# Kernel tuning notes

Hardware: AMD Instinct MI355X
Metric: run time of the kernel (lower is better)

Reference implementation:

```python
import jax, jax.numpy as jnp
import numpy as np

SCALE = 10.0
TEMP = 0.5
SIM_TH = 0.7
EPOCH = 1
KL_WEIGHT = max(0.5 * (1 - EPOCH / 60), 0.1)
NEG_INF = -1e30


def _normalize(x, eps=1e-12):
    n = jnp.linalg.norm(x, axis=-1, keepdims=True)
    return x / jnp.maximum(n, eps)


def setup_inputs() -> dict:
    key = jax.random.key(0)
    ks = jax.random.split(key, 6)
    P, B, D, N, K = 4, 128, 512, 32768, 10
    # 0.02 scale keeps pairwise distances O(1) so exp(-SCALE*dist) does not underflow
    feature = jax.random.normal(ks[0], (P, B, D), jnp.float32) * 0.02
    text_feature = jax.random.normal(ks[1], (B, P, D), jnp.float32) * 0.02
    centers = jax.random.normal(ks[2], (P, N, D), jnp.float32) * 0.02
    position = jax.random.randint(ks[3], (B,), 0, N)
    cross_indices = jax.random.randint(ks[4], (B, K), 0, N)
    vid = jax.random.randint(ks[5], (N,), 0, 751)
    return {"feature": feature, "text_feature": text_feature, "centers": centers,
            "position": position, "cross_indices": cross_indices, "vid": vid}


def _align_loss(feature, text_feature):
    # feature: [P,B,D]; text_feature: [B,P,D] (detached in original)
    img = _normalize(feature)
    txt = _normalize(jax.lax.stop_gradient(jnp.transpose(text_feature, (1, 0, 2))))
    img_sim = jnp.einsum('pbd,pcd->pbc', img, img) / TEMP   # [P,B,B]
    txt_sim = jnp.einsum('pbd,pcd->pbc', txt, txt) / TEMP
    mask = (img_sim > SIM_TH) & (txt_sim > SIM_TH)
    valid = mask.any(-1)                                   # [P,B] row/col validity
    colm = valid[:, None, :]                               # mask over columns
    il = jnp.where(colm, img_sim, NEG_INF)
    tl = jnp.where(colm, txt_sim, NEG_INF)
    img_logp = jax.nn.log_softmax(il, -1)
    txt_logp = jax.nn.log_softmax(tl, -1)                  # fully detached (txt detached)
    txt_prob = jnp.exp(txt_logp)
    img_logp_sg = jax.lax.stop_gradient(img_logp)
    img_prob = jnp.exp(img_logp_sg)
    # F.kl_div(input=log q, target=p) = sum p*(log p - log q), batchmean over valid rows
    kl1 = jnp.sum(jnp.where(colm, txt_prob * (txt_logp - img_logp), 0.0), -1)      # [P,B]
    kl2 = jnp.sum(jnp.where(colm, img_prob * (img_logp_sg - txt_logp), 0.0), -1)
    nvalid = valid.sum(-1)                                 # [P]
    r1 = jnp.sum(jnp.where(valid, kl1, 0.0), -1)
    r2 = jnp.sum(jnp.where(valid, kl2, 0.0), -1)
    per_part = 0.5 * (r1 + r2) / jnp.maximum(nvalid, 1)
    return jnp.sum(jnp.where(nvalid > 0, per_part, 0.0))


def _contrastive_loss(feature, centers, position, cross_indices):
    P, B, D = feature.shape
    N = centers.shape[1]
    pos_feats = jnp.take(centers, cross_indices, axis=1)   # [P,B,K,D]
    fn2 = jnp.sum(feature * feature, -1)                   # [P,B]
    pn2 = jnp.sum(pos_feats * pos_feats, -1)               # [P,B,K]
    pd2 = fn2[..., None] + pn2 - 2.0 * jnp.einsum('pbd,pbkd->pbk', feature, pos_feats)
    pos_dist = jnp.sqrt(jnp.maximum(pd2, 1e-12))           # [P,B,K]
    cn2 = jnp.sum(centers * centers, -1)                   # [P,N]
    nd2 = fn2[..., None] + cn2[:, None, :] - 2.0 * jnp.einsum('pbd,pnd->pbn', feature, centers)
    neg_dist = jnp.sqrt(jnp.maximum(nd2, 1e-12))           # [P,B,N]
    neg_mask = (jnp.ones((N,), bool)
                .at[cross_indices.reshape(-1)].set(False)
                .at[position].set(False))
    x = jnp.log(jnp.sum(jnp.exp(-SCALE * pos_dist), -1))   # [P,B]
    ey = jnp.exp(-SCALE * neg_dist) * neg_mask[None, None, :].astype(neg_dist.dtype)
    y = jnp.log(jnp.sum(ey, -1))                           # [P,B]
    l = jnp.sum(y - x, -1) / B                             # per-part, div by feature.size(1)
    l = jnp.where(jnp.isnan(l), 0.0, l)
    return jnp.sum(l) / P


def reference(feature, text_feature, centers, position, cross_indices, vid):
    align_loss = _align_loss(feature, text_feature)
    contrastive_loss = _contrastive_loss(feature, centers, position, cross_indices)
    total_loss = contrastive_loss + KL_WEIGHT * align_loss
    pos_vid = jnp.take(vid, cross_indices, axis=0)         # [B,K]
    return total_loss, contrastive_loss, align_loss, pos_vid
```

## Files before the change

### kernel.cpp

```cpp
#include <hip/hip_runtime.h>
#include <hip/hip_bf16.h>
#include <math.h>

#define P_ 4
#define B_ 128
#define D_ 512
#define N_ 32768
#define K_ 10
#define TNB 128
#define NT2 (N_ / TNB)
#define BK2 32
#define NCH (D_ / BK2)
#define KP2 42

typedef __attribute__((ext_vector_type(8))) short bf16x8;
typedef __attribute__((ext_vector_type(4))) float f32x4;

#define LDS_BARRIER() asm volatile("s_waitcnt lgkmcnt(0)\n\ts_barrier" ::: "memory")

static __device__ __forceinline__ float block_sum_128(float v, float* sh) {
    const int t = threadIdx.x;
    sh[t] = v; __syncthreads();
    #pragma unroll
    for (int s = 64; s > 0; s >>= 1) { if (t < s) sh[t] += sh[t + s]; __syncthreads(); }
    float r = sh[0]; __syncthreads();
    return r;
}

static __device__ __forceinline__ uint2 pack_bf16x4(float4 v) {
    union { __hip_bfloat162 h; unsigned u; } lo, hi;
    lo.h = __float22bfloat162_rn(make_float2(v.x, v.y));
    hi.h = __float22bfloat162_rn(make_float2(v.z, v.w));
    uint2 r; r.x = lo.u; r.y = hi.u;
    return r;
}

__global__ __launch_bounds__(256) void prep_kernel(const float* __restrict__ feature,
                                                   unsigned short* __restrict__ Abf,
                                                   float* __restrict__ fn2) {
    const int pb = blockIdx.x;
    const int t = threadIdx.x;
    const float2 v = *(const float2*)(feature + (size_t)pb * D_ + 2 * t);
    union { __hip_bfloat162 h; unsigned u; } pk;
    pk.h = __float22bfloat162_rn(make_float2(v.x, v.y));
    ((unsigned*)Abf)[(size_t)pb * (D_ / 2) + t] = pk.u;
    __shared__ float sred[256];
    sred[t] = v.x * v.x + v.y * v.y;
    __syncthreads();
    #pragma unroll
    for (int s = 128; s > 0; s >>= 1) { if (t < s) sred[t] += sred[t + s]; __syncthreads(); }
    if (t == 0) fn2[pb] = sred[0];
}

__global__ __launch_bounds__(128) void sim_kernel(
    const float* __restrict__ feature,
    const float* __restrict__ text_feature,
    float* __restrict__ img_sim,
    float* __restrict__ txt_sim,
    float* __restrict__ validf,
    float* __restrict__ Ssum) {
    const int p = blockIdx.x;
    const int b0 = blockIdx.y * 2;
    const int c = threadIdx.x;
    if (blockIdx.y == 0) Ssum[p * B_ + c] = 0.0f;
    __shared__ float ai[2][D_];
    __shared__ float at[2][D_];
    __shared__ float cinv_i[128];
    __shared__ float cinv_t[128];
    __shared__ int flags[2];
    #pragma unroll
    for (int i = 0; i < 8; ++i) {
        int idx = c + i * 128;
        int row = idx >> 9, d = idx & 511;
        ai[row][d] = feature[(size_t)(p * B_ + b0 + row) * D_ + d];
        at[row][d] = text_feature[((size_t)(b0 + row) * P_ + p) * D_ + d];
    }
    if (c < 2) flags[c] = 0;
    __syncthreads();
    float di[2] = {0, 0};
    float dt[2] = {0, 0};
    float ssi = 0.0f, sst = 0.0f;
    const float* fc = feature + (size_t)(p * B_ + c) * D_;
    const float* tc = text_feature + ((size_t)c * P_ + p) * D_;
    for (int d = 0; d < D_; d += 4) {
        float4 vi = *(const float4*)(fc + d);
        float4 vt = *(const float4*)(tc + d);
        ssi += vi.x * vi.x + vi.y * vi.y + vi.z * vi.z + vi.w * vi.w;
        sst += vt.x * vt.x + vt.y * vt.y + vt.z * vt.z + vt.w * vt.w;
        #pragma unroll
        for (int i = 0; i < 2; ++i) {
            float4 a4 = *(const float4*)&ai[i][d];
            float4 t4 = *(const float4*)&at[i][d];
            di[i] += a4.x * vi.x + a4.y * vi.y + a4.z * vi.z + a4.w * vi.w;
            dt[i] += t4.x * vt.x + t4.y * vt.y + t4.z * vt.z + t4.w * vt.w;
        }
    }
    cinv_i[c] = 1.0f / fmaxf(sqrtf(ssi), 1e-12f);
    cinv_t[c] = 1.0f / fmaxf(sqrtf(sst), 1e-12f);
    __syncthreads();
    #pragma unroll
    for (int i = 0; i < 2; ++i) {
        float is = 2.0f * di[i] * cinv_i[b0 + i] * cinv_i[c];
        float ts = 2.0f * dt[i] * cinv_t[b0 + i] * cinv_t[c];
        img_sim[(size_t)(p * B_ + b0 + i) * B_ + c] = is;
        txt_sim[(size_t)(p * B_ + b0 + i) * B_ + c] = ts;
        if (is > 0.7f && ts > 0.7f) flags[i] = 1;
    }
    __syncthreads();
    if (c < 2) validf[p * B_ + b0 + c] = (float)flags[c];
}

__global__ __launch_bounds__(256) void kl_kernel(
    const float* __restrict__ img_sim,
    const float* __restrict__ txt_sim,
    const float* __restrict__ validf,
    float* __restrict__ klrow) {
    const int l = threadIdx.x & 63;
    const int wv = threadIdx.x >> 6;
    const int p = blockIdx.x;
    const int r = blockIdx.y * 4 + wv;
    const size_t base = (size_t)(p * B_ + r) * B_;
    const bool v0 = validf[p * B_ + l] > 0.5f;
    const bool v1 = validf[p * B_ + 64 + l] > 0.5f;
    const float il0 = v0 ? img_sim[base + l] : -1e30f;
    const float il1 = v1 ? img_sim[base + 64 + l] : -1e30f;
    const float tl0 = v0 ? txt_sim[base + l] : -1e30f;
    const float tl1 = v1 ? txt_sim[base + 64 + l] : -1e30f;
    float mi = fmaxf(il0, il1), mt = fmaxf(tl0, tl1);
    #pragma unroll
    for (int off = 32; off > 0; off >>= 1) {
        mi = fmaxf(mi, __shfl_xor(mi, off));
        mt = fmaxf(mt, __shfl_xor(mt, off));
    }
    float si = expf(il0 - mi) + expf(il1 - mi);
    float st = expf(tl0 - mt) + expf(tl1 - mt);
    #pragma unroll
    for (int off = 32; off > 0; off >>= 1) {
        si += __shfl_xor(si, off);
        st += __shfl_xor(st, off);
    }
    const float lsei = mi + logf(si);
    const float lset = mt + logf(st);
    float term = 0.0f;
    if (v0) {
        float lpi = il0 - lsei, lpt = tl0 - lset;
        term += expf(lpt) * (lpt - lpi) + expf(lpi) * (lpi - lpt);
    }
    if (v1) {
        float lpi = il1 - lsei, lpt = tl1 - lset;
        term += expf(lpt) * (lpt - lpi) + expf(lpi) * (lpi - lpt);
    }
    #pragma unroll
    for (int off = 32; off > 0; off >>= 1) term += __shfl_xor(term, off);
    if (l == 0) klrow[p * B_ + r] = (validf[p * B_ + r] > 0.5f) ? term : 0.0f;
}

__global__ void posx_kernel(const float* __restrict__ feature,
                            const float* __restrict__ centers,
                            const int* __restrict__ cross,
                            float* __restrict__ xarr) {
    const int pb = blockIdx.x;
    const int p = pb >> 7, b = pb & 127;
    const int l = threadIdx.x;
    const float* f = feature + (size_t)pb * D_;
    float4 f0 = *(const float4*)(f + l * 4);
    float4 f1 = *(const float4*)(f + 256 + l * 4);
    float fs = f0.x * f0.x + f0.y * f0.y + f0.z * f0.z + f0.w * f0.w
             + f1.x * f1.x + f1.y * f1.y + f1.z * f1.z + f1.w * f1.w;
    #pragma unroll
    for (int off = 32; off > 0; off >>= 1) fs += __shfl_down(fs, off);
    float ex = 0.0f;
    #pragma unroll
    for (int k = 0; k < K_; ++k) {
        int idx = cross[b * K_ + k];
        const float* cp = centers + ((size_t)p * N_ + idx) * D_;
        float4 c0 = *(const float4*)(cp + l * 4);
        float4 c1 = *(const float4*)(cp + 256 + l * 4);
        float dot = f0.x * c0.x + f0.y * c0.y + f0.z * c0.z + f0.w * c0.w
                  + f1.x * c1.x + f1.y * c1.y + f1.z * c1.z + f1.w * c1.w;
        float pn2 = c0.x * c0.x + c0.y * c0.y + c0.z * c0.z + c0.w * c0.w
                  + c1.x * c1.x + c1.y * c1.y + c1.z * c1.z + c1.w * c1.w;
        #pragma unroll
        for (int off = 32; off > 0; off >>= 1) {
            dot += __shfl_down(dot, off);
            pn2 += __shfl_down(pn2, off);
        }
        if (l == 0) {
            float d2 = fs + pn2 - 2.0f * dot;
            ex += expf(-10.0f * sqrtf(fmaxf(d2, 1e-12f)));
        }
    }
    if (l == 0) xarr[pb] = logf(ex);
}

__global__ __launch_bounds__(256) void neg_mfma_kernel(
    const unsigned short* __restrict__ Abf,
    const float* __restrict__ centers,
    const float* __restrict__ fn2,
    const int* __restrict__ cross,
    const int* __restrict__ position,
    float* __restrict__ Ssum) {
    const int tile = blockIdx.x;
    const int p = blockIdx.y;
    const int n0g = tile * TNB;
    const int t = threadIdx.x;
    const int l = t & 63;
    const int w = t >> 6;
    const int m0w = (w & 1) * 64;
    const int n0w = (w >> 1) * 64;

    __shared__ unsigned short Bs[2][128 * KP2];
    __shared__ float cn2s[128];
    __shared__ float fn2s[128];
    __shared__ float red[128];
    __shared__ float msk[128];

    if (t < 128) { red[t] = 0.0f; msk[t] = 1.0f; fn2s[t] = fn2[p * B_ + t]; }

    f32x4 acc[4][4];
    #pragma unroll
    for (int i = 0; i < 4; ++i)
        #pragma unroll
        for (int j = 0; j < 4; ++j) acc[i][j] = (f32x4)0.0f;

    float c2acc[4] = {0.0f, 0.0f, 0.0f, 0.0f};

    const float* Bb = centers + ((size_t)p * N_ + n0g) * D_;

    const int f8 = t & 7;
    const int r0 = t >> 3;

    const int ko = (l >> 4) * 8;
    const int fr = l & 15;
    const unsigned short* Afr = Abf + ((size_t)p * B_ + m0w + fr) * D_ + ko;

    float4 vb[4];
    bf16x8 afc[4], afn[4];

    #pragma unroll
    for (int i = 0; i < 4; ++i)
        vb[i] = *(const float4*)(Bb + (size_t)(r0 + 32 * i) * D_ + f8 * 4);
    #pragma unroll
    for (int i = 0; i < 4; ++i)
        afc[i] = *(const bf16x8*)(Afr + (size_t)(i * 16) * D_);
    #pragma unroll
    for (int i = 0; i < 4; ++i) {
        const int row = r0 + 32 * i;
        *(uint2*)&Bs[0][row * KP2 + f8 * 4] = pack_bf16x4(vb[i]);
        c2acc[i] += vb[i].x * vb[i].x + vb[i].y * vb[i].y
                  + vb[i].z * vb[i].z + vb[i].w * vb[i].w;
    }
    LDS_BARRIER();

    for (int i = t; i < B_ * K_ + B_; i += 256) {
        const int v = (i < B_ * K_) ? cross[i] : position[i - B_ * K_];
        const unsigned rr = (unsigned)(v - n0g);
        if (rr < (unsigned)TNB) msk[rr] = 0.0f;
    }

    #pragma unroll 2
    for (int c = 0; c < NCH; ++c) {
        const int cur = c & 1;
        if (c + 1 < NCH) {
            const int kk = (c + 1) * BK2;
            #pragma unroll
            for (int i = 0; i < 4; ++i)
                vb[i] = *(const float4*)(Bb + (size_t)(r0 + 32 * i) * D_ + kk + f8 * 4);
            #pragma unroll
            for (int i = 0; i < 4; ++i)
                afn[i] = *(const bf16x8*)(Afr + (size_t)(i * 16) * D_ + kk);
        }
        bf16x8 bfr[4];
        #pragma unroll
        for (int i = 0; i < 4; ++i)
            bfr[i] = *(const bf16x8*)&Bs[cur][(n0w + i * 16 + fr) * KP2 + ko];
        #pragma unroll
        for (int i = 0; i < 4; ++i)
            #pragma unroll
            for (int j = 0; j < 4; ++j)
                acc[i][j] = __builtin_amdgcn_mfma_f32_16x16x32_bf16(
                    afc[i], bfr[j], acc[i][j], 0, 0, 0);
        if (c + 1 < NCH) {
            #pragma unroll
            for (int i = 0; i < 4; ++i) {
                const int row = r0 + 32 * i;
                *(uint2*)&Bs[cur ^ 1][row * KP2 + f8 * 4] = pack_bf16x4(vb[i]);
                c2acc[i] += vb[i].x * vb[i].x + vb[i].y * vb[i].y
                          + vb[i].z * vb[i].z + vb[i].w * vb[i].w;
            }
        }
        LDS_BARRIER();
        #pragma unroll
        for (int i = 0; i < 4; ++i) afc[i] = afn[i];
    }

    #pragma unroll
    for (int i = 0; i < 4; ++i) {
        float s = c2acc[i];
        s += __shfl_xor(s, 1); s += __shfl_xor(s, 2); s += __shfl_xor(s, 4);
        if (f8 == 0) cn2s[r0 + 32 * i] = s;
    }
    LDS_BARRIER();

    float c2l[4], mkl[4];
    #pragma unroll
    for (int j = 0; j < 4; ++j) {
        const int col = n0w + j * 16 + fr;
        c2l[j] = cn2s[col];
        mkl[j] = msk[col];
    }
    #pragma unroll
    for (int i = 0; i < 4; ++i) {
        #pragma unroll
        for (int r = 0; r < 4; ++r) {
            const int row = m0w + i * 16 + (l >> 4) * 4 + r;
            const float fv = fn2s[row];
            float s = 0.0f;
            #pragma unroll
            for (int j = 0; j < 4; ++j) {
                const float nd2 = fv + c2l[j] - 2.0f * acc[i][j][r];
                s += mkl[j] * __expf(-10.0f * sqrtf(fmaxf(nd2, 1e-12f)));
            }
            s += __shfl_xor(s, 1); s += __shfl_xor(s, 2);
            s += __shfl_xor(s, 4); s += __shfl_xor(s, 8);
            if (fr == 0) atomicAdd(&red[row], s);
        }
    }
    LDS_BARRIER();
    if (t < 128) atomicAdd(&Ssum[p * B_ + t], red[t]);
}

__global__ void final_kernel(const float* __restrict__ validf,
                             const float* __restrict__ klrow,
                             const float* __restrict__ xarr,
                             const float* __restrict__ Ssum,
                             const int* __restrict__ cross,
                             const int* __restrict__ vid,
                             float* __restrict__ out) {
    const int t = threadIdx.x;
    __shared__ float sh[128];
    __shared__ float accum[2];
    if (t == 0) { accum[0] = 0.0f; accum[1] = 0.0f; }
    __syncthreads();
    for (int p = 0; p < P_; ++p) {
        float nv = block_sum_128(validf[p * B_ + t], sh);
        float ks = block_sum_128(klrow[p * B_ + t], sh);
        float dv = logf(Ssum[p * B_ + t]) - xarr[p * B_ + t];
        float ds = block_sum_128(dv, sh);
        if (t == 0) {
            float lp = ds / (float)B_;
            if (!(lp != lp)) accum[0] += lp;
            if (nv > 0.5f) accum[1] += 0.5f * ks / fmaxf(nv, 1.0f);
        }
        __syncthreads();
    }
    if (t == 0) {
        float contrastive = accum[0] / (float)P_;
        float align = accum[1];
        out[1] = contrastive;
        out[2] = align;
        out[0] = contrastive + 0.49166666666666664f * align;
    }
    #pragma unroll
    for (int k = 0; k < K_; ++k) {
        const int i = k * 128 + t;
        out[3 + i] = (float)vid[cross[i]];
    }
}

extern "C" void kernel_launch(void* const* d_in, const int* in_sizes, int n_in,
                              void* d_out, int out_size, void* d_ws, size_t ws_size,
                              hipStream_t stream) {
    const float* feature      = (const float*)d_in[0];
    const float* text_feature = (const float*)d_in[1];
    const float* centers      = (const float*)d_in[2];
    const int*   position     = (const int*)d_in[3];
    const int*   cross        = (const int*)d_in[4];
    const int*   vid          = (const int*)d_in[5];
    float* out = (float*)d_out;

    float* ws      = (float*)d_ws;
    float* img_sim = ws;
    float* txt_sim = img_sim + (size_t)P_ * B_ * B_;
    float* validf  = txt_sim + (size_t)P_ * B_ * B_;
    float* klrow   = validf + P_ * B_;
    float* xarr    = klrow + P_ * B_;
    float* Ssum    = xarr + P_ * B_;
    float* fn2     = Ssum + P_ * B_;
    unsigned short* Abf = (unsigned short*)(fn2 + P_ * B_);

    prep_kernel<<<P_ * B_, 256, 0, stream>>>(feature, Abf, fn2);
    sim_kernel<<<dim3(P_, B_ / 2), 128, 0, stream>>>(feature, text_feature,
                                                     img_sim, txt_sim, validf, Ssum);
    kl_kernel<<<dim3(P_, B_ / 4), 256, 0, stream>>>(img_sim, txt_sim, validf, klrow);
    posx_kernel<<<P_ * B_, 64, 0, stream>>>(feature, centers, cross, xarr);
    neg_mfma_kernel<<<dim3(NT2, P_), 256, 0, stream>>>(Abf, centers, fn2, cross,
                                                       position, Ssum);
    final_kernel<<<1, 128, 0, stream>>>(validf, klrow, xarr, Ssum, cross, vid, out);
}
```

Baseline: 452.9 us.

## Load centers directly into MFMA fragments, dropping LDS staging and barriers

The neg_mfma_kernel no longer stages the fp32 centers tile through a double-buffered LDS bf16 buffer. Each lane now loads its own B fragment straight from global memory, converts it to bf16 in registers and computes the center squared norms locally with cross-lane shuffles. The main loop is restructured into two register sets that are manually ping-ponged, removing the per-chunk LDS barriers. In exchange, each pair of waves sharing the same column tile loads that B data redundantly, so global/L2 traffic rises, and the per-lane loads are strided rows of 32 bytes, which may coalesce worse.

```diff
diff --git a/kernel.cpp b/kernel.cpp
--- a/kernel.cpp
+++ b/kernel.cpp
@@ -11,12 +11,9 @@
 #define NT2 (N_ / TNB)
 #define BK2 32
 #define NCH (D_ / BK2)
-#define KP2 42
 
 typedef __attribute__((ext_vector_type(8))) short bf16x8;
 typedef __attribute__((ext_vector_type(4))) float f32x4;
-
-#define LDS_BARRIER() asm volatile("s_waitcnt lgkmcnt(0)\n\ts_barrier" ::: "memory")
 
 static __device__ __forceinline__ float block_sum_128(float v, float* sh) {
     const int t = threadIdx.x;
@@ -193,6 +190,44 @@
     if (l == 0) xarr[pb] = logf(ex);
 }
 
+static __device__ __forceinline__ void load_set(
+    const unsigned short* Ap, const float* Bp, int kk,
+    bf16x8 (&aX)[4], float4 (&b0X)[4], float4 (&b1X)[4]) {
+    #pragma unroll
+    for (int i = 0; i < 4; ++i)
+        aX[i] = *(const bf16x8*)(Ap + (size_t)(i * 16) * D_ + kk);
+    #pragma unroll
+    for (int j = 0; j < 4; ++j) {
+        const float* r = Bp + (size_t)(j * 16) * D_ + kk;
+        b0X[j] = *(const float4*)(r);
+        b1X[j] = *(const float4*)(r + 4);
+    }
+}
+
+static __device__ __forceinline__ void compute_set(
+    const bf16x8 (&aX)[4], const float4 (&b0X)[4], const float4 (&b1X)[4],
+    f32x4 (&acc)[4][4], float (&cn2p)[4]) {
+    bf16x8 bfr[4];
+    #pragma unroll
+    for (int j = 0; j < 4; ++j) {
+        cn2p[j] += b0X[j].x * b0X[j].x + b0X[j].y * b0X[j].y
+                 + b0X[j].z * b0X[j].z + b0X[j].w * b0X[j].w
+                 + b1X[j].x * b1X[j].x + b1X[j].y * b1X[j].y
+                 + b1X[j].z * b1X[j].z + b1X[j].w * b1X[j].w;
+        uint2 lo = pack_bf16x4(b0X[j]);
+        uint2 hi = pack_bf16x4(b1X[j]);
+        union { unsigned u[4]; bf16x8 v; } m;
+        m.u[0] = lo.x; m.u[1] = lo.y; m.u[2] = hi.x; m.u[3] = hi.y;
+        bfr[j] = m.v;
+    }
+    #pragma unroll
+    for (int i = 0; i < 4; ++i)
+        #pragma unroll
+        for (int j = 0; j < 4; ++j)
+            acc[i][j] = __builtin_amdgcn_mfma_f32_16x16x32_bf16(
+                aX[i], bfr[j], acc[i][j], 0, 0, 0);
+}
+
 __global__ __launch_bounds__(256) void neg_mfma_kernel(
     const unsigned short* __restrict__ Abf,
     const float* __restrict__ centers,
@@ -209,111 +244,58 @@
     const int m0w = (w & 1) * 64;
     const int n0w = (w >> 1) * 64;
 
-    __shared__ unsigned short Bs[2][128 * KP2];
-    __shared__ float cn2s[128];
-    __shared__ float fn2s[128];
     __shared__ float red[128];
     __shared__ float msk[128];
+    __shared__ float fn2s[128];
 
     if (t < 128) { red[t] = 0.0f; msk[t] = 1.0f; fn2s[t] = fn2[p * B_ + t]; }
-
-    f32x4 acc[4][4];
-    #pragma unroll
-    for (int i = 0; i < 4; ++i)
-        #pragma unroll
-        for (int j = 0; j < 4; ++j) acc[i][j] = (f32x4)0.0f;
-
-    float c2acc[4] = {0.0f, 0.0f, 0.0f, 0.0f};
-
-    const float* Bb = centers + ((size_t)p * N_ + n0g) * D_;
-
-    const int f8 = t & 7;
-    const int r0 = t >> 3;
-
-    const int ko = (l >> 4) * 8;
-    const int fr = l & 15;
-    const unsigned short* Afr = Abf + ((size_t)p * B_ + m0w + fr) * D_ + ko;
-
-    float4 vb[4];
-    bf16x8 afc[4], afn[4];
-
-    #pragma unroll
-    for (int i = 0; i < 4; ++i)
-        vb[i] = *(const float4*)(Bb + (size_t)(r0 + 32 * i) * D_ + f8 * 4);
-    #pragma unroll
-    for (int i = 0; i < 4; ++i)
-        afc[i] = *(const bf16x8*)(Afr + (size_t)(i * 16) * D_);
-    #pragma unroll
-    for (int i = 0; i < 4; ++i) {
-        const int row = r0 + 32 * i;
-        *(uint2*)&Bs[0][row * KP2 + f8 * 4] = pack_bf16x4(vb[i]);
-        c2acc[i] += vb[i].x * vb[i].x + vb[i].y * vb[i].y
-                  + vb[i].z * vb[i].z + vb[i].w * vb[i].w;
-    }
-    LDS_BARRIER();
-
+    __syncthreads();
     for (int i = t; i < B_ * K_ + B_; i += 256) {
         const int v = (i < B_ * K_) ? cross[i] : position[i - B_ * K_];
         const unsigned rr = (unsigned)(v - n0g);
         if (rr < (unsigned)TNB) msk[rr] = 0.0f;
     }
-
-    #pragma unroll 2
-    for (int c = 0; c < NCH; ++c) {
-        const int cur = c & 1;
-        if (c + 1 < NCH) {
-            const int kk = (c + 1) * BK2;
-            #pragma unroll
-            for (int i = 0; i < 4; ++i)
-                vb[i] = *(const float4*)(Bb + (size_t)(r0 + 32 * i) * D_ + kk + f8 * 4);
-            #pragma unroll
-            for (int i = 0; i < 4; ++i)
-                afn[i] = *(const bf16x8*)(Afr + (size_t)(i * 16) * D_ + kk);
-        }
-        bf16x8 bfr[4];
-        #pragma unroll
-        for (int i = 0; i < 4; ++i)
-            bfr[i] = *(const bf16x8*)&Bs[cur][(n0w + i * 16 + fr) * KP2 + ko];
-        #pragma unroll
-        for (int i = 0; i < 4; ++i)
-            #pragma unroll
-            for (int j = 0; j < 4; ++j)
-                acc[i][j] = __builtin_amdgcn_mfma_f32_16x16x32_bf16(
-                    afc[i], bfr[j], acc[i][j], 0, 0, 0);
-        if (c + 1 < NCH) {
-            #pragma unroll
-            for (int i = 0; i < 4; ++i) {
-                const int row = r0 + 32 * i;
-                *(uint2*)&Bs[cur ^ 1][row * KP2 + f8 * 4] = pack_bf16x4(vb[i]);
-                c2acc[i] += vb[i].x * vb[i].x + vb[i].y * vb[i].y
-                          + vb[i].z * vb[i].z + vb[i].w * vb[i].w;
-            }
-        }
-        LDS_BARRIER();
-        #pragma unroll
-        for (int i = 0; i < 4; ++i) afc[i] = afn[i];
+    __syncthreads();
+
+    const int fr = l & 15;
+    const int kg = l >> 4;
+    const unsigned short* Ap = Abf + ((size_t)p * B_ + m0w + fr) * D_ + kg * 8;
+    const float* Bp = centers + ((size_t)p * N_ + n0g + n0w + fr) * D_ + kg * 8;
+
+    f32x4 acc[4][4];
+    #pragma unroll
+    for (int i = 0; i < 4; ++i)
+        #pragma unroll
+        for (int j = 0; j < 4; ++j) acc[i][j] = (f32x4)0.0f;
+    float cn2p[4] = {0.0f, 0.0f, 0.0f, 0.0f};
+
+    bf16x8 aA[4], aB[4];
+    float4 b0A[4], b1A[4], b0B[4], b1B[4];
+
+    load_set(Ap, Bp, 0, aA, b0A, b1A);
+    #pragma unroll 1
+    for (int c = 0; c < NCH; c += 2) {
+        load_set(Ap, Bp, (c + 1) * BK2, aB, b0B, b1B);
+        compute_set(aA, b0A, b1A, acc, cn2p);
+        if (c + 2 < NCH) load_set(Ap, Bp, (c + 2) * BK2, aA, b0A, b1A);
+        compute_set(aB, b0B, b1B, acc, cn2p);
+    }
+
+    float c2l[4], mkl[4];
+    #pragma unroll
+    for (int j = 0; j < 4; ++j) {
+        float s = cn2p[j];
+        s += __shfl_xor(s, 16);
+        s += __shfl_xor(s, 32);
+        c2l[j] = s;
+        mkl[j] = msk[n0w + j * 16 + fr];
     }
 
     #pragma unroll
     for (int i = 0; i < 4; ++i) {
-        float s = c2acc[i];
-        s += __shfl_xor(s, 1); s += __shfl_xor(s, 2); s += __shfl_xor(s, 4);
-        if (f8 == 0) cn2s[r0 + 32 * i] = s;
-    }
-    LDS_BARRIER();
-
-    float c2l[4], mkl[4];
-    #pragma unroll
-    for (int j = 0; j < 4; ++j) {
-        const int col = n0w + j * 16 + fr;
-        c2l[j] = cn2s[col];
-        mkl[j] = msk[col];
-    }
-    #pragma unroll
-    for (int i = 0; i < 4; ++i) {
         #pragma unroll
         for (int r = 0; r < 4; ++r) {
-            const int row = m0w + i * 16 + (l >> 4) * 4 + r;
+            const int row = m0w + i * 16 + kg * 4 + r;
             const float fv = fn2s[row];
             float s = 0.0f;
             #pragma unroll
@@ -326,7 +308,7 @@
             if (fr == 0) atomicAdd(&red[row], s);
         }
     }
-    LDS_BARRIER();
+    __syncthreads();
     if (t < 128) atomicAdd(&Ssum[p * B_ + t], red[t]);
 }
 
```

After: 457.3 us. Within noise of the previous version (+1.0%).
